# Performance work log

Measured on AMD Instinct MI355X. Metric: run time of the kernel, lower is better.

## Reference

```python
import jax, jax.numpy as jnp
import numpy as np

IMG = 512
STRIDES = (8.0, 16.0, 32.0)   # p3, p4, p5
ROI = 7                        # roi_size
SR = 2                         # roi_align sampling ratio (fixed; torchvision default -1 is adaptive)
IOU_LOW, IOU_HIGH = 0.4, 0.6   # fg/bg matching thresholds (2nd-stage)
NUM_CLASSES = 20
B, R, M, C = 4, 256, 40, 256


def _make_boxes(key, b, n, max_wh):
    k1, k2 = jax.random.split(key)
    cxy = jax.random.uniform(k1, (b, n, 2), minval=0.0, maxval=float(IMG))
    wh = jax.random.uniform(k2, (b, n, 2), minval=16.0, maxval=float(max_wh))
    x1y1 = jnp.clip(cxy - wh / 2, 0.0, IMG - 1.0)
    x2y2 = jnp.clip(cxy + wh / 2, x1y1 + 1.0, float(IMG))
    return jnp.concatenate([x1y1, x2y2], axis=-1)


def setup_inputs() -> dict:
    key = jax.random.key(0)
    ks = jax.random.split(key, 12)
    feats_p3 = jax.random.normal(ks[0], (B, C, 64, 64), jnp.float32)
    feats_p4 = jax.random.normal(ks[1], (B, C, 32, 32), jnp.float32)
    feats_p5 = jax.random.normal(ks[2], (B, C, 16, 16), jnp.float32)
    props_p3 = _make_boxes(ks[3], B, R, 128)
    props_p4 = _make_boxes(ks[4], B, R, 256)
    props_p5 = _make_boxes(ks[5], B, R, 512)
    gt_xyxy = _make_boxes(ks[6], B, M, 400)
    gt_cls = jax.random.randint(ks[7], (B, M, 1), 0, NUM_CLASSES).astype(jnp.float32)
    gt = jnp.concatenate([gt_xyxy, gt_cls], axis=-1)
    pad = (jnp.arange(M) >= 25)[None, :, None]   # last 15 rows are padding (class -1)
    gt_boxes = jnp.where(pad, -1.0, gt)
    conv_w = jax.random.normal(ks[8], (C, C, 3, 3), jnp.float32) * 0.01
    conv_b = jnp.zeros((C,), jnp.float32)
    fc_w = jax.random.normal(ks[9], (NUM_CLASSES + 1, C * ROI * ROI), jnp.float32) * 0.01
    fc_b = jnp.zeros((NUM_CLASSES + 1,), jnp.float32)
    return {"feats_p3": feats_p3, "feats_p4": feats_p4, "feats_p5": feats_p5,
            "props_p3": props_p3, "props_p4": props_p4, "props_p5": props_p5,
            "gt_boxes": gt_boxes, "conv_w": conv_w, "conv_b": conv_b,
            "fc_w": fc_w, "fc_b": fc_b}


def _bilinear(feat, ys, xs):
    # feat: (C,H,W); ys: (R,G,1); xs: (R,1,G) -> (C,R,G,G)
    Cc, H, W = feat.shape
    valid = (ys >= -1.0) & (ys <= H) & (xs >= -1.0) & (xs <= W)
    y = jnp.clip(ys, 0.0, H - 1.0)
    x = jnp.clip(xs, 0.0, W - 1.0)
    y0f = jnp.floor(y); x0f = jnp.floor(x)
    y0 = y0f.astype(jnp.int32); x0 = x0f.astype(jnp.int32)
    y1 = jnp.minimum(y0 + 1, H - 1); x1 = jnp.minimum(x0 + 1, W - 1)
    ly = y - y0f; lx = x - x0f
    hy = 1.0 - ly; hx = 1.0 - lx
    v = (feat[:, y0, x0] * (hy * hx) + feat[:, y0, x1] * (hy * lx)
         + feat[:, y1, x0] * (ly * hx) + feat[:, y1, x1] * (ly * lx))
    return jnp.where(valid, v, 0.0)


def _roi_align(feat, rois, scale):
    # feat: (C,H,W); rois: (R,4) xyxy in image coords; aligned=True
    r = rois.shape[0]
    x1 = rois[:, 0] * scale - 0.5
    y1 = rois[:, 1] * scale - 0.5
    roi_w = rois[:, 2] * scale - 0.5 - x1
    roi_h = rois[:, 3] * scale - 0.5 - y1
    G = ROI * SR
    frac = (jnp.arange(G, dtype=feat.dtype) + 0.5) / G
    xs = x1[:, None] + frac[None, :] * roi_w[:, None]   # (R,G)
    ys = y1[:, None] + frac[None, :] * roi_h[:, None]
    v = _bilinear(feat, ys[:, :, None], xs[:, None, :])  # (C,R,G,G)
    v = v.transpose(1, 0, 2, 3).reshape(r, -1, ROI, SR, ROI, SR)
    return v.mean(axis=(3, 5))                            # (R,C,7,7)


def _iou(b1, b2):
    # b1: (N,4), b2: (M,4) -> (N,M)
    tl = jnp.maximum(b1[:, None, :2], b2[None, :, :2])
    br = jnp.minimum(b1[:, None, 2:4], b2[None, :, 2:4])
    inter = jnp.clip(br - tl, 0.0).prod(-1)
    a1 = (b1[:, 2:4] - b1[:, :2]).prod(-1)
    a2 = (b2[:, 2:4] - b2[:, :2]).prod(-1)
    return inter / (a1[:, None] + a2[None, :] - inter)


def _match(props, gt):
    # props: (N,4); gt: (M,5) padded with class -1
    valid = gt[:, 4] != -1
    m = jnp.where(valid[None, :], _iou(props, gt[:, :4]), -1.0)
    q = m.max(axis=1)
    matched = gt[m.argmax(axis=1)]                       # (N,5)
    matched = jnp.where((q <= IOU_LOW)[:, None], -1.0, matched)      # background
    matched = jnp.where(((q > IOU_LOW) & (q < IOU_HIGH))[:, None], -1e8, matched)  # neutral
    return matched


def reference(feats_p3, feats_p4, feats_p5, props_p3, props_p4, props_p5,
              gt_boxes, conv_w, conv_b, fc_w, fc_b):
    levels = [(feats_p3, props_p3, STRIDES[0]),
              (feats_p4, props_p4, STRIDES[1]),
              (feats_p5, props_p5, STRIDES[2])]
    # ROI-align every proposal at its level; order: image-major, then level, then roi
    per_level = [jax.vmap(lambda f, p, s=s: _roi_align(f, p, 1.0 / s))(f, p)
                 for f, p, s in levels]                   # each (B,R,C,7,7)
    roi_feats = jnp.stack(per_level, axis=1).reshape(-1, C, ROI, ROI)
    # cls head: conv3x3 + relu + flatten + linear
    h = jax.lax.conv_general_dilated(roi_feats, conv_w, (1, 1), 'SAME')
    h = jax.nn.relu(h + conv_b[None, :, None, None])
    logits = h.reshape(h.shape[0], -1) @ fc_w.T + fc_b    # (B*3*R, num_classes+1)
    # match concatenated per-image proposals to GT (no-grad pipeline)
    props_all = jnp.concatenate([props_p3, props_p4, props_p5], axis=1)  # (B,3R,4)
    matched = jax.vmap(_match)(jax.lax.stop_gradient(props_all), gt_boxes)
    return logits, matched
```

## Files before the change

### kernel.cpp

```cpp
#include <hip/hip_runtime.h>

typedef unsigned short ushort_t;
typedef __attribute__((ext_vector_type(4))) unsigned short ushort4_t;
typedef __attribute__((ext_vector_type(8))) short short8;
typedef __attribute__((ext_vector_type(4))) unsigned int uint4v;
typedef __attribute__((ext_vector_type(2))) float float2v;
typedef __attribute__((ext_vector_type(4))) float floatx4;
typedef __attribute__((ext_vector_type(16))) float floatx16;

#define B_ 4
#define C_ 256
#define R_ 256
#define M_ 40
#define NCLS 21
#define ROI_ 7
#define G_ 14
#define NROI_TOT 3072
#define PROPS_PER_IMG 768
#define POOL_PITCH 264
#define WCONV_ELEMS (256 * 2304)
#define NKB 392
#define WFC2_ELEMS (NKB * 32 * 32)
#define OFF_FWB   WCONV_ELEMS
#define OFF_CL3   (OFF_FWB + WFC2_ELEMS)
#define OFF_CL4   (OFF_CL3 + 4 * 64 * 64 * 256)
#define OFF_CL5   (OFF_CL4 + 4 * 32 * 32 * 256)

__device__ __forceinline__ ushort_t f2bf(float f) {
  unsigned u = __builtin_bit_cast(unsigned, f);
  u += 0x7fff + ((u >> 16) & 1);
  return (ushort_t)(u >> 16);
}
__device__ __forceinline__ float bf2f(ushort_t h) {
  unsigned u = ((unsigned)h) << 16;
  return __builtin_bit_cast(float, u);
}
__device__ __forceinline__ float2v cvt2(unsigned u) {
  float2v r;
  r[0] = __builtin_bit_cast(float, u << 16);
  r[1] = __builtin_bit_cast(float, u & 0xffff0000u);
  return r;
}

template <int W>
__device__ __forceinline__ void transpose_feat(const float* __restrict__ in,
                                               ushort_t* __restrict__ outp,
                                               const int fid, const int t,
                                               ushort_t* __restrict__ tile) {
  const int b = fid / W;
  const int y = fid - b * W;
  const float* src = in + (size_t)(b * 256) * (W * W) + (size_t)y * W;
#pragma unroll
  for (int i = 0; i < W / 4; ++i) {
    const int f4 = t + i * 256;
    const int c = f4 / (W / 4);
    const int x = (f4 - c * (W / 4)) * 4;
    const floatx4 v = *(const floatx4*)(src + (size_t)c * (W * W) + x);
    tile[c * 65 + x + 0] = f2bf(v[0]);
    tile[c * 65 + x + 1] = f2bf(v[1]);
    tile[c * 65 + x + 2] = f2bf(v[2]);
    tile[c * 65 + x + 3] = f2bf(v[3]);
  }
  __syncthreads();
  ushort_t* orow = outp + ((size_t)(b * W + y) * W) * 256;
#pragma unroll
  for (int i = 0; i < W / 4; ++i) {
    const int idx = t + i * 256;
    const int x = idx >> 6;
    const int c4 = (idx & 63) * 4;
    ushort4_t v;
    v[0] = tile[(c4 + 0) * 65 + x];
    v[1] = tile[(c4 + 1) * 65 + x];
    v[2] = tile[(c4 + 2) * 65 + x];
    v[3] = tile[(c4 + 3) * 65 + x];
    *(ushort4_t*)(orow + (size_t)x * 256 + c4) = v;
  }
}

__global__ __launch_bounds__(256) void prep_kernel(
    const float* __restrict__ cw, const float* __restrict__ fw,
    const float* __restrict__ f3, const float* __restrict__ f4,
    const float* __restrict__ f5, const float* __restrict__ p3,
    const float* __restrict__ p4, const float* __restrict__ p5,
    const float* __restrict__ gt, ushort_t* __restrict__ wr,
    ushort_t* __restrict__ fwb, ushort_t* __restrict__ cl3,
    ushort_t* __restrict__ cl4, ushort_t* __restrict__ cl5,
    float* __restrict__ out) {
  __shared__ ushort_t tile[256 * 65];
  const int id = blockIdx.x;
  const int t = threadIdx.x;

  if (id < 512) {
    const int i0 = id * 256 + t;
    const int stride = 512 * 256;
    for (int idx = i0; idx < WCONV_ELEMS; idx += stride) {
      const int kk = idx >> 12;
      const int rem = idx & 4095;
      const int co = rem >> 4;
      const int i = rem & 15;
      const int k = kk * 16 + i;
      const int j = k >> 8;
      const int ci = k & 255;
      wr[idx] = f2bf(cw[(co * 256 + ci) * 9 + j]);
    }
    for (int idx = i0; idx < WFC2_ELEMS; idx += stride) {
      const int kb = idx >> 10;
      const int rem = idx & 1023;
      const int cls = rem >> 5;
      const int koff = rem & 31;
      fwb[idx] =
          (cls < NCLS) ? f2bf(fw[(size_t)cls * 12544 + kb * 32 + koff]) : 0;
    }
  } else if (id < 960) {
    const int fid = id - 512;
    if (fid < 256)      transpose_feat<64>(f3, cl3, fid, t, tile);
    else if (fid < 384) transpose_feat<32>(f4, cl4, fid - 256, t, tile);
    else                transpose_feat<16>(f5, cl5, fid - 384, t, tile);
  } else {
    const int gidx = (id - 960) * 256 + t;
    if (gidx >= NROI_TOT) return;
    const int b = gidx / PROPS_PER_IMG;
    const int i = gidx - b * PROPS_PER_IMG;
    const int lvl = i >> 8;
    const int r = i & 255;
    const float* prop =
        (lvl == 0 ? p3 : (lvl == 1 ? p4 : p5)) + (size_t)(b * R_ + r) * 4;
    const float px1 = prop[0], py1 = prop[1], px2 = prop[2], py2 = prop[3];
    const float a1 = (px2 - px1) * (py2 - py1);
    const float* gtb = gt + (size_t)b * M_ * 5;

    float best = -2.f;
    int bi = 0;
    for (int j = 0; j < M_; ++j) {
      const float gx1 = gtb[j * 5 + 0], gy1 = gtb[j * 5 + 1];
      const float gx2 = gtb[j * 5 + 2], gy2 = gtb[j * 5 + 3];
      const float cls = gtb[j * 5 + 4];
      const float tlx = fmaxf(px1, gx1), tly = fmaxf(py1, gy1);
      const float brx = fminf(px2, gx2), bry = fminf(py2, gy2);
      const float iw = fmaxf(brx - tlx, 0.f), ih = fmaxf(bry - tly, 0.f);
      const float inter = iw * ih;
      const float a2 = (gx2 - gx1) * (gy2 - gy1);
      const float iou = inter / ((a1 + a2) - inter);
      const float m = (cls != -1.0f) ? iou : -1.0f;
      if (m > best) { best = m; bi = j; }
    }
    float o0, o1, o2, o3, o4;
    if (best <= 0.4f) {
      o0 = o1 = o2 = o3 = o4 = -1.0f;
    } else if (best < 0.6f) {
      o0 = o1 = o2 = o3 = o4 = -1e8f;
    } else {
      o0 = gtb[bi * 5 + 0]; o1 = gtb[bi * 5 + 1]; o2 = gtb[bi * 5 + 2];
      o3 = gtb[bi * 5 + 3]; o4 = gtb[bi * 5 + 4];
    }
    float* od = out + (size_t)NROI_TOT * NCLS + (size_t)gidx * 5;
    od[0] = o0; od[1] = o1; od[2] = o2; od[3] = o3; od[4] = o4;
  }
}

__global__ __launch_bounds__(512, 4) void cls_head_kernel(
    const ushort_t* __restrict__ cl3, const ushort_t* __restrict__ cl4,
    const ushort_t* __restrict__ cl5, const float* __restrict__ p3,
    const float* __restrict__ p4, const float* __restrict__ p5,
    const ushort_t* __restrict__ wr, const float* __restrict__ conv_b,
    const ushort_t* __restrict__ fwb, const float* __restrict__ fc_b,
    float* __restrict__ out) {
  __shared__ __align__(16) ushort_t s_pool[2 * 50 * POOL_PITCH];
  __shared__ int s_iy0[28], s_iy1[28], s_ix0[28], s_ix1[28];
  __shared__ float s_ly[28], s_lx[28], s_vy[28], s_vx[28];
  __shared__ float s_fcred[NCLS * 2 * 8];

  const int bid = blockIdx.x;
  const int t = threadIdx.x;

  const int img = (bid & 7) >> 1;
  const int pair = (bid >> 3) * 2 + (bid & 1);
  const int rid0 = img * PROPS_PER_IMG + pair * 2;

  const ushort_t* clb_[2];
  int W_[2];
  const float* prop_[2];
#pragma unroll
  for (int rr = 0; rr < 2; ++rr) {
    const int rid = rid0 + rr;
    const int b = rid / PROPS_PER_IMG;
    const int rem = rid - b * PROPS_PER_IMG;
    const int lvl = rem >> 8;
    const int r = rem & 255;
    const ushort_t* base;
    const float* pp;
    int Wl;
    if (lvl == 0) { base = cl3; pp = p3; Wl = 64; }
    else if (lvl == 1) { base = cl4; pp = p4; Wl = 32; }
    else { base = cl5; pp = p5; Wl = 16; }
    clb_[rr] = base + (size_t)b * Wl * Wl * 256;
    W_[rr] = Wl;
    prop_[rr] = pp + (size_t)(b * R_ + r) * 4;
  }

  if (t < 256) {
    s_pool[49 * POOL_PITCH + t] = 0;
    s_pool[99 * POOL_PITCH + t] = 0;
  }

  if (t < 56) {
    const int rr = t / 28;
    const int tt = t - rr * 28;
    const float* prop = prop_[rr];
    const int H = W_[rr];
    const float scale = 1.0f / (float)(H == 64 ? 8 : (H == 32 ? 16 : 32));
    const float bx1 = prop[0], by1 = prop[1], bx2 = prop[2], by2 = prop[3];
    const float ax = bx1 * scale - 0.5f;
    const float ay = by1 * scale - 0.5f;
    const float rw = bx2 * scale - 0.5f - ax;
    const float rh = by2 * scale - 0.5f - ay;
    const int i = (tt < G_) ? tt : (tt - G_);
    const float frac = ((float)i + 0.5f) / (float)G_;
    const int o = rr * G_ + i;
    if (tt < G_) {
      float yy = ay + frac * rh;
      float v = (yy >= -1.0f && yy <= (float)H) ? 1.0f : 0.0f;
      float y = fminf(fmaxf(yy, 0.0f), (float)(H - 1));
      float y0f = floorf(y);
      int y0 = (int)y0f;
      s_iy0[o] = y0;
      s_iy1[o] = min(y0 + 1, H - 1);
      s_ly[o] = y - y0f;
      s_vy[o] = v;
    } else {
      float xx = ax + frac * rw;
      float v = (xx >= -1.0f && xx <= (float)H) ? 1.0f : 0.0f;
      float x = fminf(fmaxf(xx, 0.0f), (float)(H - 1));
      float x0f = floorf(x);
      int x0 = (int)x0f;
      s_ix0[o] = x0;
      s_ix1[o] = min(x0 + 1, H - 1);
      s_lx[o] = x - x0f;
      s_vx[o] = v;
    }
  }
  __syncthreads();

  const int l = t & 63;
  const int w = t >> 6;

  {
    const int hw = l >> 5;
    const int c8 = (l & 31) * 8;
    for (int cb = w * 2; cb < 98; cb += 16) {
      const int cell = cb + hw;
      if (cell >= 98) continue;
      const int rr = (cell >= 49) ? 1 : 0;
      const int pos = cell - rr * 49;
      const int py = pos / 7, px = pos - (pos / 7) * 7;
      const ushort_t* clb = clb_[rr];
      const int W = W_[rr];
      float2v a01 = {0.f, 0.f}, a23 = {0.f, 0.f};
      float2v a45 = {0.f, 0.f}, a67 = {0.f, 0.f};
#pragma unroll
      for (int sy = 0; sy < 2; ++sy) {
        const int gy = rr * G_ + 2 * py + sy;
        const int iy0 = s_iy0[gy], iy1 = s_iy1[gy];
        const float ly = s_ly[gy], vy = s_vy[gy];
        const float hy = 1.0f - ly;
#pragma unroll
        for (int sx = 0; sx < 2; ++sx) {
          const int gx = rr * G_ + 2 * px + sx;
          const int ix0 = s_ix0[gx], ix1 = s_ix1[gx];
          const float lx = s_lx[gx], vx = s_vx[gx];
          const float hx = 1.0f - lx;
          const float vv = vy * vx;
          const float w00 = vv * hy * hx, w01 = vv * hy * lx;
          const float w10 = vv * ly * hx, w11 = vv * ly * lx;
          const uint4v u00 = *(const uint4v*)(clb + ((size_t)(iy0 * W + ix0) * 256 + c8));
          const uint4v u01 = *(const uint4v*)(clb + ((size_t)(iy0 * W + ix1) * 256 + c8));
          const uint4v u10 = *(const uint4v*)(clb + ((size_t)(iy1 * W + ix0) * 256 + c8));
          const uint4v u11 = *(const uint4v*)(clb + ((size_t)(iy1 * W + ix1) * 256 + c8));
          a01 += cvt2(u00[0]) * w00 + cvt2(u01[0]) * w01 +
                 cvt2(u10[0]) * w10 + cvt2(u11[0]) * w11;
          a23 += cvt2(u00[1]) * w00 + cvt2(u01[1]) * w01 +
                 cvt2(u10[1]) * w10 + cvt2(u11[1]) * w11;
          a45 += cvt2(u00[2]) * w00 + cvt2(u01[2]) * w01 +
                 cvt2(u10[2]) * w10 + cvt2(u11[2]) * w11;
          a67 += cvt2(u00[3]) * w00 + cvt2(u01[3]) * w01 +
                 cvt2(u10[3]) * w10 + cvt2(u11[3]) * w11;
        }
      }
      short8 pv;
      pv[0] = (short)f2bf(a01[0] * 0.25f);
      pv[1] = (short)f2bf(a01[1] * 0.25f);
      pv[2] = (short)f2bf(a23[0] * 0.25f);
      pv[3] = (short)f2bf(a23[1] * 0.25f);
      pv[4] = (short)f2bf(a45[0] * 0.25f);
      pv[5] = (short)f2bf(a45[1] * 0.25f);
      pv[6] = (short)f2bf(a67[0] * 0.25f);
      pv[7] = (short)f2bf(a67[1] * 0.25f);
      *(short8*)&s_pool[(rr * 50 + pos) * POOL_PITCH + c8] = pv;
    }
  }
  __syncthreads();

  const int ml = l & 31;
  const int quad = l >> 5;
  const int co_base = w * 32;

  const int pA = ml;
  const int pB = ml + 32;
  const int pyA = pA / 7, pxA = pA % 7;
  const int pyB = pB / 7, pxB = pB % 7;

  floatx16 acc[4];
#pragma unroll
  for (int a = 0; a < 4; ++a)
#pragma unroll
    for (int i = 0; i < 16; ++i) acc[a][i] = 0.f;

  const ushort_t* a0p = wr + (co_base + ml) * 16 + quad * 8;

  __builtin_amdgcn_s_setprio(1);
  int kk = 0;
  for (int j = 0; j < 9; ++j) {
    const int dy = j / 3 - 1, dx = j % 3 - 1;
    int bnA, bnB;
    {
      const int ry = pyA + dy, rx = pxA + dx;
      const bool ok = (ry >= 0) & (ry < 7) & (rx >= 0) & (rx < 7);
      bnA = ok ? ry * 7 + rx : 49;
    }
    {
      const int ry = pyB + dy, rx = pxB + dx;
      const bool ok = (pB < 49) & (ry >= 0) & (ry < 7) & (rx >= 0) & (rx < 7);
      bnB = ok ? ry * 7 + rx : 49;
    }
    const int row0 = bnA, row1 = bnB, row2 = 50 + bnA, row3 = 50 + bnB;

#pragma unroll 4
    for (int kc = 0; kc < 16; ++kc, ++kk) {
      const short8 a0 = *(const short8*)(a0p + kk * 4096);
      const int cof = kc * 16 + quad * 8;
      const short8 b0 = *(const short8*)&s_pool[row0 * POOL_PITCH + cof];
      const short8 b1 = *(const short8*)&s_pool[row1 * POOL_PITCH + cof];
      const short8 b2 = *(const short8*)&s_pool[row2 * POOL_PITCH + cof];
      const short8 b3 = *(const short8*)&s_pool[row3 * POOL_PITCH + cof];
      acc[0] = __builtin_amdgcn_mfma_f32_32x32x16_bf16(a0, b0, acc[0], 0, 0, 0);
      acc[1] = __builtin_amdgcn_mfma_f32_32x32x16_bf16(a0, b1, acc[1], 0, 0, 0);
      acc[2] = __builtin_amdgcn_mfma_f32_32x32x16_bf16(a0, b2, acc[2], 0, 0, 0);
      acc[3] = __builtin_amdgcn_mfma_f32_32x32x16_bf16(a0, b3, acc[3], 0, 0, 0);
    }
  }
  __builtin_amdgcn_s_setprio(0);
  __syncthreads();

  ushort_t* h_lds = s_pool;
#pragma unroll
  for (int reg = 0; reg < 16; ++reg) {
    const int co = co_base + (reg & 3) + 8 * (reg >> 2) + 4 * quad;
    const float cb = conv_b[co];
    const int base = co * 49;
    h_lds[base + pA] = f2bf(fmaxf(acc[0][reg] + cb, 0.f));
    h_lds[12544 + base + pA] = f2bf(fmaxf(acc[2][reg] + cb, 0.f));
    if (pB < 49) {
      h_lds[base + pB] = f2bf(fmaxf(acc[1][reg] + cb, 0.f));
      h_lds[12544 + base + pB] = f2bf(fmaxf(acc[3][reg] + cb, 0.f));
    }
  }
  __syncthreads();

  {
    const int n = l & 15;
    const int kq = l >> 4;
    const ushort_t* ap0 = fwb + (n * 4 + kq) * 8;
    const ushort_t* ap1 = ap0 + 512;
    const ushort_t* bp = h_lds + (size_t)(l & 1) * 12544 + kq * 8;
    const int kb0 = w * 49;

    floatx4 fa0, fa1;
#pragma unroll
    for (int i = 0; i < 4; ++i) { fa0[i] = 0.f; fa1[i] = 0.f; }

    for (int it = 0; it < 49; ++it) {
      const int kb = kb0 + it;
      const short8 av0 = *(const short8*)(ap0 + kb * 1024);
      const short8 av1 = *(const short8*)(ap1 + kb * 1024);
      const short8 bv = *(const short8*)(bp + kb * 32);
      fa0 = __builtin_amdgcn_mfma_f32_16x16x32_bf16(av0, bv, fa0, 0, 0, 0);
      fa1 = __builtin_amdgcn_mfma_f32_16x16x32_bf16(av1, bv, fa1, 0, 0, 0);
    }
    if (n < 2) {
      const int m4 = kq * 4;
#pragma unroll
      for (int reg = 0; reg < 4; ++reg) {
        const int cls0 = m4 + reg;
        const int cls1 = 16 + m4 + reg;
        s_fcred[(cls0 * 2 + n) * 8 + w] = fa0[reg];
        if (cls1 < NCLS) s_fcred[(cls1 * 2 + n) * 8 + w] = fa1[reg];
      }
    }
  }
  __syncthreads();
  if (t < 2 * NCLS) {
    const int cls = t >> 1;
    const int rr = t & 1;
    const float* pr = &s_fcred[(cls * 2 + rr) * 8];
    float s = pr[0] + pr[1] + pr[2] + pr[3] + pr[4] + pr[5] + pr[6] + pr[7];
    out[(size_t)(rid0 + rr) * NCLS + cls] = s + fc_b[cls];
  }
}

extern "C" void kernel_launch(void* const* d_in, const int* in_sizes, int n_in,
                              void* d_out, int out_size, void* d_ws,
                              size_t ws_size, hipStream_t stream) {
  const float* f3 = (const float*)d_in[0];
  const float* f4 = (const float*)d_in[1];
  const float* f5 = (const float*)d_in[2];
  const float* p3 = (const float*)d_in[3];
  const float* p4 = (const float*)d_in[4];
  const float* p5 = (const float*)d_in[5];
  const float* gt = (const float*)d_in[6];
  const float* cw = (const float*)d_in[7];
  const float* cb = (const float*)d_in[8];
  const float* fw = (const float*)d_in[9];
  const float* fb = (const float*)d_in[10];
  float* out = (float*)d_out;

  ushort_t* wsp = (ushort_t*)d_ws;
  ushort_t* wr = wsp;
  ushort_t* fwb = wsp + OFF_FWB;
  ushort_t* cl3 = wsp + OFF_CL3;
  ushort_t* cl4 = wsp + OFF_CL4;
  ushort_t* cl5 = wsp + OFF_CL5;

  prep_kernel<<<972, 256, 0, stream>>>(cw, fw, f3, f4, f5, p3, p4, p5, gt, wr,
                                       fwb, cl3, cl4, cl5, out);
  cls_head_kernel<<<NROI_TOT / 2, 512, 0, stream>>>(cl3, cl4, cl5, p3, p4, p5,
                                                    wr, cb, fwb, fb, out);
}
```

Before: 360.1 us.

## Process three ROIs per block to amortize conv weight loads

Each block of the fused ROI-align, conv and FC head now handles three ROIs instead of two. The conv MFMA loop tiles 147 output positions into five 32-column tiles in place of four tiles over two separately padded ROIs. Every conv weight fragment fetched from global memory is therefore reused across more ROI positions, and the grid shrinks to 1024 blocks. The trade-offs are more LDS and accumulator registers per block, possibly lower occupancy, and dropping the s_setprio hint.

Result: faster. 319.0 us (-11.4%).

```diff
diff --git a/kernel.cpp b/kernel.cpp
--- a/kernel.cpp
+++ b/kernel.cpp
@@ -18,6 +18,7 @@
 #define NROI_TOT 3072
 #define PROPS_PER_IMG 768
 #define POOL_PITCH 264
+#define POOL_ROWS 148
 #define WCONV_ELEMS (256 * 2304)
 #define NKB 392
 #define WFC2_ELEMS (NKB * 32 * 32)
@@ -30,10 +31,6 @@
   unsigned u = __builtin_bit_cast(unsigned, f);
   u += 0x7fff + ((u >> 16) & 1);
   return (ushort_t)(u >> 16);
-}
-__device__ __forceinline__ float bf2f(ushort_t h) {
-  unsigned u = ((unsigned)h) << 16;
-  return __builtin_bit_cast(float, u);
 }
 __device__ __forceinline__ float2v cvt2(unsigned u) {
   float2v r;
@@ -165,26 +162,28 @@
     const ushort_t* __restrict__ wr, const float* __restrict__ conv_b,
     const ushort_t* __restrict__ fwb, const float* __restrict__ fc_b,
     float* __restrict__ out) {
-  __shared__ __align__(16) ushort_t s_pool[2 * 50 * POOL_PITCH];
-  __shared__ int s_iy0[28], s_iy1[28], s_ix0[28], s_ix1[28];
-  __shared__ float s_ly[28], s_lx[28], s_vy[28], s_vx[28];
-  __shared__ float s_fcred[NCLS * 2 * 8];
+  __shared__ __align__(16) ushort_t s_pool[POOL_ROWS * POOL_PITCH];
+  __shared__ union SU {
+    struct {
+      int iy0[42], iy1[42], ix0[42], ix1[42];
+      float ly[42], lx[42], vy[42], vx[42];
+    } tb;
+    float fcred[NCLS * 3 * 8];
+  } s_u;
 
   const int bid = blockIdx.x;
   const int t = threadIdx.x;
 
   const int img = (bid & 7) >> 1;
-  const int pair = (bid >> 3) * 2 + (bid & 1);
-  const int rid0 = img * PROPS_PER_IMG + pair * 2;
-
-  const ushort_t* clb_[2];
-  int W_[2];
-  const float* prop_[2];
-#pragma unroll
-  for (int rr = 0; rr < 2; ++rr) {
-    const int rid = rid0 + rr;
-    const int b = rid / PROPS_PER_IMG;
-    const int rem = rid - b * PROPS_PER_IMG;
+  const int grp = (bid >> 3) * 2 + (bid & 1);
+  const int rid0 = img * PROPS_PER_IMG + grp * 3;
+
+  const ushort_t *clb0, *clb1, *clb2;
+  const float *pr0, *pr1, *pr2;
+  int W0, W1, W2;
+#pragma unroll
+  for (int rr = 0; rr < 3; ++rr) {
+    const int rem = grp * 3 + rr;
     const int lvl = rem >> 8;
     const int r = rem & 255;
     const ushort_t* base;
@@ -193,21 +192,20 @@
     if (lvl == 0) { base = cl3; pp = p3; Wl = 64; }
     else if (lvl == 1) { base = cl4; pp = p4; Wl = 32; }
     else { base = cl5; pp = p5; Wl = 16; }
-    clb_[rr] = base + (size_t)b * Wl * Wl * 256;
-    W_[rr] = Wl;
-    prop_[rr] = pp + (size_t)(b * R_ + r) * 4;
-  }
-
-  if (t < 256) {
-    s_pool[49 * POOL_PITCH + t] = 0;
-    s_pool[99 * POOL_PITCH + t] = 0;
-  }
-
-  if (t < 56) {
+    base += (size_t)img * Wl * Wl * 256;
+    pp += (size_t)(img * R_ + r) * 4;
+    if (rr == 0) { clb0 = base; pr0 = pp; W0 = Wl; }
+    else if (rr == 1) { clb1 = base; pr1 = pp; W1 = Wl; }
+    else { clb2 = base; pr2 = pp; W2 = Wl; }
+  }
+
+  if (t < POOL_PITCH) s_pool[147 * POOL_PITCH + t] = 0;
+
+  if (t < 84) {
     const int rr = t / 28;
     const int tt = t - rr * 28;
-    const float* prop = prop_[rr];
-    const int H = W_[rr];
+    const float* prop = rr == 0 ? pr0 : (rr == 1 ? pr1 : pr2);
+    const int H = rr == 0 ? W0 : (rr == 1 ? W1 : W2);
     const float scale = 1.0f / (float)(H == 64 ? 8 : (H == 32 ? 16 : 32));
     const float bx1 = prop[0], by1 = prop[1], bx2 = prop[2], by2 = prop[3];
     const float ax = bx1 * scale - 0.5f;
@@ -223,20 +221,20 @@
       float y = fminf(fmaxf(yy, 0.0f), (float)(H - 1));
       float y0f = floorf(y);
       int y0 = (int)y0f;
-      s_iy0[o] = y0;
-      s_iy1[o] = min(y0 + 1, H - 1);
-      s_ly[o] = y - y0f;
-      s_vy[o] = v;
+      s_u.tb.iy0[o] = y0;
+      s_u.tb.iy1[o] = min(y0 + 1, H - 1);
+      s_u.tb.ly[o] = y - y0f;
+      s_u.tb.vy[o] = v;
     } else {
       float xx = ax + frac * rw;
       float v = (xx >= -1.0f && xx <= (float)H) ? 1.0f : 0.0f;
       float x = fminf(fmaxf(xx, 0.0f), (float)(H - 1));
       float x0f = floorf(x);
       int x0 = (int)x0f;
-      s_ix0[o] = x0;
-      s_ix1[o] = min(x0 + 1, H - 1);
-      s_lx[o] = x - x0f;
-      s_vx[o] = v;
+      s_u.tb.ix0[o] = x0;
+      s_u.tb.ix1[o] = min(x0 + 1, H - 1);
+      s_u.tb.lx[o] = x - x0f;
+      s_u.tb.vx[o] = v;
     }
   }
   __syncthreads();
@@ -247,27 +245,27 @@
   {
     const int hw = l >> 5;
     const int c8 = (l & 31) * 8;
-    for (int cb = w * 2; cb < 98; cb += 16) {
+    for (int cb = w * 2; cb < 147; cb += 16) {
       const int cell = cb + hw;
-      if (cell >= 98) continue;
-      const int rr = (cell >= 49) ? 1 : 0;
+      if (cell >= 147) continue;
+      const int rr = (cell >= 98) ? 2 : ((cell >= 49) ? 1 : 0);
       const int pos = cell - rr * 49;
       const int py = pos / 7, px = pos - (pos / 7) * 7;
-      const ushort_t* clb = clb_[rr];
-      const int W = W_[rr];
+      const ushort_t* clb = rr == 0 ? clb0 : (rr == 1 ? clb1 : clb2);
+      const int W = rr == 0 ? W0 : (rr == 1 ? W1 : W2);
       float2v a01 = {0.f, 0.f}, a23 = {0.f, 0.f};
       float2v a45 = {0.f, 0.f}, a67 = {0.f, 0.f};
 #pragma unroll
       for (int sy = 0; sy < 2; ++sy) {
         const int gy = rr * G_ + 2 * py + sy;
-        const int iy0 = s_iy0[gy], iy1 = s_iy1[gy];
-        const float ly = s_ly[gy], vy = s_vy[gy];
+        const int iy0 = s_u.tb.iy0[gy], iy1 = s_u.tb.iy1[gy];
+        const float ly = s_u.tb.ly[gy], vy = s_u.tb.vy[gy];
         const float hy = 1.0f - ly;
 #pragma unroll
         for (int sx = 0; sx < 2; ++sx) {
           const int gx = rr * G_ + 2 * px + sx;
-          const int ix0 = s_ix0[gx], ix1 = s_ix1[gx];
-          const float lx = s_lx[gx], vx = s_vx[gx];
+          const int ix0 = s_u.tb.ix0[gx], ix1 = s_u.tb.ix1[gx];
+          const float lx = s_u.tb.lx[gx], vx = s_u.tb.vx[gx];
           const float hx = 1.0f - lx;
           const float vv = vy * vx;
           const float w00 = vv * hy * hx, w01 = vv * hy * lx;
@@ -295,7 +293,7 @@
       pv[5] = (short)f2bf(a45[1] * 0.25f);
       pv[6] = (short)f2bf(a67[0] * 0.25f);
       pv[7] = (short)f2bf(a67[1] * 0.25f);
-      *(short8*)&s_pool[(rr * 50 + pos) * POOL_PITCH + c8] = pv;
+      *(short8*)&s_pool[cell * POOL_PITCH + c8] = pv;
     }
   }
   __syncthreads();
@@ -304,64 +302,68 @@
   const int quad = l >> 5;
   const int co_base = w * 32;
 
-  const int pA = ml;
-  const int pB = ml + 32;
-  const int pyA = pA / 7, pxA = pA % 7;
-  const int pyB = pB / 7, pxB = pB % 7;
-
-  floatx16 acc[4];
-#pragma unroll
-  for (int a = 0; a < 4; ++a)
+  int gp_[5], py_[5], px_[5];
+  bool ok_[5];
+#pragma unroll
+  for (int tt = 0; tt < 5; ++tt) {
+    const int gp = tt * 32 + ml;
+    gp_[tt] = gp;
+    ok_[tt] = gp < 147;
+    const int rr = (gp >= 98) ? 2 : ((gp >= 49) ? 1 : 0);
+    const int pos = gp - rr * 49;
+    py_[tt] = pos / 7;
+    px_[tt] = pos - (pos / 7) * 7;
+  }
+
+  floatx16 acc[5];
+#pragma unroll
+  for (int a = 0; a < 5; ++a)
 #pragma unroll
     for (int i = 0; i < 16; ++i) acc[a][i] = 0.f;
 
   const ushort_t* a0p = wr + (co_base + ml) * 16 + quad * 8;
 
-  __builtin_amdgcn_s_setprio(1);
   int kk = 0;
   for (int j = 0; j < 9; ++j) {
     const int dy = j / 3 - 1, dx = j % 3 - 1;
-    int bnA, bnB;
-    {
-      const int ry = pyA + dy, rx = pxA + dx;
-      const bool ok = (ry >= 0) & (ry < 7) & (rx >= 0) & (rx < 7);
-      bnA = ok ? ry * 7 + rx : 49;
-    }
-    {
-      const int ry = pyB + dy, rx = pxB + dx;
-      const bool ok = (pB < 49) & (ry >= 0) & (ry < 7) & (rx >= 0) & (rx < 7);
-      bnB = ok ? ry * 7 + rx : 49;
-    }
-    const int row0 = bnA, row1 = bnB, row2 = 50 + bnA, row3 = 50 + bnB;
+    int bn[5];
+#pragma unroll
+    for (int tt = 0; tt < 5; ++tt) {
+      const int ry = py_[tt] + dy, rx = px_[tt] + dx;
+      const bool okn = ok_[tt] & (ry >= 0) & (ry < 7) & (rx >= 0) & (rx < 7);
+      bn[tt] = okn ? gp_[tt] + dy * 7 + dx : 147;
+    }
 
 #pragma unroll 4
     for (int kc = 0; kc < 16; ++kc, ++kk) {
       const short8 a0 = *(const short8*)(a0p + kk * 4096);
       const int cof = kc * 16 + quad * 8;
-      const short8 b0 = *(const short8*)&s_pool[row0 * POOL_PITCH + cof];
-      const short8 b1 = *(const short8*)&s_pool[row1 * POOL_PITCH + cof];
-      const short8 b2 = *(const short8*)&s_pool[row2 * POOL_PITCH + cof];
-      const short8 b3 = *(const short8*)&s_pool[row3 * POOL_PITCH + cof];
-      acc[0] = __builtin_amdgcn_mfma_f32_32x32x16_bf16(a0, b0, acc[0], 0, 0, 0);
-      acc[1] = __builtin_amdgcn_mfma_f32_32x32x16_bf16(a0, b1, acc[1], 0, 0, 0);
-      acc[2] = __builtin_amdgcn_mfma_f32_32x32x16_bf16(a0, b2, acc[2], 0, 0, 0);
-      acc[3] = __builtin_amdgcn_mfma_f32_32x32x16_bf16(a0, b3, acc[3], 0, 0, 0);
-    }
-  }
-  __builtin_amdgcn_s_setprio(0);
+#pragma unroll
+      for (int tt = 0; tt < 5; ++tt) {
+        const short8 bv = *(const short8*)&s_pool[bn[tt] * POOL_PITCH + cof];
+        acc[tt] =
+            __builtin_amdgcn_mfma_f32_32x32x16_bf16(a0, bv, acc[tt], 0, 0, 0);
+      }
+    }
+  }
   __syncthreads();
 
   ushort_t* h_lds = s_pool;
-#pragma unroll
-  for (int reg = 0; reg < 16; ++reg) {
-    const int co = co_base + (reg & 3) + 8 * (reg >> 2) + 4 * quad;
-    const float cb = conv_b[co];
-    const int base = co * 49;
-    h_lds[base + pA] = f2bf(fmaxf(acc[0][reg] + cb, 0.f));
-    h_lds[12544 + base + pA] = f2bf(fmaxf(acc[2][reg] + cb, 0.f));
-    if (pB < 49) {
-      h_lds[base + pB] = f2bf(fmaxf(acc[1][reg] + cb, 0.f));
-      h_lds[12544 + base + pB] = f2bf(fmaxf(acc[3][reg] + cb, 0.f));
+  float cbv[16];
+#pragma unroll
+  for (int reg = 0; reg < 16; ++reg)
+    cbv[reg] = conv_b[co_base + (reg & 3) + 8 * (reg >> 2) + 4 * quad];
+#pragma unroll
+  for (int tt = 0; tt < 5; ++tt) {
+    if (ok_[tt]) {
+      const int gp = gp_[tt];
+      const int rr = (gp >= 98) ? 2 : ((gp >= 49) ? 1 : 0);
+      const int hbase = rr * 12544 + (gp - rr * 49);
+#pragma unroll
+      for (int reg = 0; reg < 16; ++reg) {
+        const int co = co_base + (reg & 3) + 8 * (reg >> 2) + 4 * quad;
+        h_lds[hbase + co * 49] = f2bf(fmaxf(acc[tt][reg] + cbv[reg], 0.f));
+      }
     }
   }
   __syncthreads();
@@ -371,7 +373,8 @@
     const int kq = l >> 4;
     const ushort_t* ap0 = fwb + (n * 4 + kq) * 8;
     const ushort_t* ap1 = ap0 + 512;
-    const ushort_t* bp = h_lds + (size_t)(l & 1) * 12544 + kq * 8;
+    const int rb = (n < 3) ? n : 0;
+    const ushort_t* bp = h_lds + (size_t)rb * 12544 + kq * 8;
     const int kb0 = w * 49;
 
     floatx4 fa0, fa1;
@@ -386,22 +389,22 @@
       fa0 = __builtin_amdgcn_mfma_f32_16x16x32_bf16(av0, bv, fa0, 0, 0, 0);
       fa1 = __builtin_amdgcn_mfma_f32_16x16x32_bf16(av1, bv, fa1, 0, 0, 0);
     }
-    if (n < 2) {
+    if (n < 3) {
       const int m4 = kq * 4;
 #pragma unroll
       for (int reg = 0; reg < 4; ++reg) {
         const int cls0 = m4 + reg;
         const int cls1 = 16 + m4 + reg;
-        s_fcred[(cls0 * 2 + n) * 8 + w] = fa0[reg];
-        if (cls1 < NCLS) s_fcred[(cls1 * 2 + n) * 8 + w] = fa1[reg];
+        s_u.fcred[(cls0 * 3 + n) * 8 + w] = fa0[reg];
+        if (cls1 < NCLS) s_u.fcred[(cls1 * 3 + n) * 8 + w] = fa1[reg];
       }
     }
   }
   __syncthreads();
-  if (t < 2 * NCLS) {
-    const int cls = t >> 1;
-    const int rr = t & 1;
-    const float* pr = &s_fcred[(cls * 2 + rr) * 8];
+  if (t < 3 * NCLS) {
+    const int cls = t / 3;
+    const int rr = t - cls * 3;
+    const float* pr = &s_u.fcred[(cls * 3 + rr) * 8];
     float s = pr[0] + pr[1] + pr[2] + pr[3] + pr[4] + pr[5] + pr[6] + pr[7];
     out[(size_t)(rid0 + rr) * NCLS + cls] = s + fc_b[cls];
   }
@@ -432,6 +435,6 @@
 
   prep_kernel<<<972, 256, 0, stream>>>(cw, fw, f3, f4, f5, p3, p4, p5, gt, wr,
                                        fwb, cl3, cl4, cl5, out);
-  cls_head_kernel<<<NROI_TOT / 2, 512, 0, stream>>>(cl3, cl4, cl5, p3, p4, p5,
+  cls_head_kernel<<<NROI_TOT / 3, 512, 0, stream>>>(cl3, cl4, cl5, p3, p4, p5,
                                                     wr, cb, fwb, fb, out);
 }
```
